# Performance work log

Hardware: AMD Instinct MI355X
Metric: run time of the kernel (lower is better)

## Reference

```python
import jax, jax.numpy as jnp
import numpy as np

NUM_NODES = 50000
NUM_EDGES = 800000
IN_CH = 64
OUT_CH = 64


def setup_inputs() -> dict:
    key = jax.random.key(0)
    k1, k2, k3, k4 = jax.random.split(key, 4)
    x = jax.random.normal(k1, (NUM_NODES, IN_CH), dtype=jnp.float32)
    edge_index = jax.random.randint(k2, (2, NUM_EDGES), 0, NUM_NODES, dtype=jnp.int32)
    W = jax.random.normal(k3, (IN_CH, OUT_CH), dtype=jnp.float32) * 0.05
    b = jax.random.normal(k4, (OUT_CH,), dtype=jnp.float32) * 0.05
    return {"x": x, "edge_index": edge_index, "W": W, "b": b}


def reference(x, edge_index, W, b):
    row, col = edge_index[0], edge_index[1]
    # Stage 1: in-degree of target nodes (math of one-hot sum == segment count)
    deg = jax.ops.segment_sum(jnp.ones_like(col, dtype=jnp.float32), col,
                              num_segments=NUM_NODES)
    deg_inv_sqrt = jnp.where(deg > 0, (deg + 1e-16) ** -0.5, 0.0)
    norm = deg_inv_sqrt[row] * deg_inv_sqrt[col]          # [E]
    # Stage 2+3: gather source features and scale by edge norm
    msg = norm[:, None] * x[row]                          # [E, IN_CH]
    # Stage 4: scatter-sum into target nodes (math of one-hot matmul)
    agg = jax.ops.segment_sum(msg, col, num_segments=NUM_NODES)  # [N, IN_CH]
    # Stage 5+6: linear transform + ReLU
    return jax.nn.relu(agg @ W + b)                       # [N, OUT_CH]
```

## Files before the change

kernel.cpp:

```cpp
#include <hip/hip_runtime.h>
#include <hip/hip_fp16.h>


#define C_CH 64
#define BW   128
#define BSH  7
#define MAXBUK 512
#define BIN_CHUNK 2048
#define NPB  32

__global__ void clearcur_kernel(int* __restrict__ bcur, int nbuk) {
    int i = blockIdx.x * blockDim.x + threadIdx.x;
    if (i < nbuk) bcur[i] = 0;
}

__global__ void __launch_bounds__(256)
bin_kernel(const int* __restrict__ row, const int* __restrict__ col,
           int* __restrict__ bcur, unsigned* __restrict__ epk,
           int E, int nbuk, int cap) {
    __shared__ int h[MAXBUK];
    __shared__ int rb[MAXBUK];
    __shared__ unsigned short rank[BIN_CHUNK];
    int tid = threadIdx.x;
    int e0 = blockIdx.x * BIN_CHUNK;
    int cntE = E - e0; if (cntE > BIN_CHUNK) cntE = BIN_CHUNK;

    for (int i = tid; i < nbuk; i += 256) h[i] = 0;
    __syncthreads();

    const int4* col4 = (const int4*)(col + e0);
    const int4* row4 = (const int4*)(row + e0);
    int cnt4 = cntE >> 2;
    for (int i = tid; i < cnt4; i += 256) {
        int4 c = col4[i];
        rank[4*i+0] = (unsigned short)atomicAdd(&h[c.x >> BSH], 1);
        rank[4*i+1] = (unsigned short)atomicAdd(&h[c.y >> BSH], 1);
        rank[4*i+2] = (unsigned short)atomicAdd(&h[c.z >> BSH], 1);
        rank[4*i+3] = (unsigned short)atomicAdd(&h[c.w >> BSH], 1);
    }
    for (int i = (cnt4 << 2) + tid; i < cntE; i += 256)
        rank[i] = (unsigned short)atomicAdd(&h[col[e0 + i] >> BSH], 1);
    __syncthreads();

    for (int i = tid; i < nbuk; i += 256)
        rb[i] = h[i] ? atomicAdd(&bcur[i], h[i]) : 0;
    __syncthreads();

    for (int i = tid; i < cnt4; i += 256) {
        int4 c = col4[i];
        int4 r = row4[i];
        #pragma unroll
        for (int j = 0; j < 4; ++j) {
            int cc = (j == 0) ? c.x : (j == 1) ? c.y : (j == 2) ? c.z : c.w;
            int rr = (j == 0) ? r.x : (j == 1) ? r.y : (j == 2) ? r.z : r.w;
            int bkt = cc >> BSH;
            int rel = rb[bkt] + (int)rank[4*i+j];
            if (rel < cap)
                epk[bkt * cap + rel] = ((unsigned)(cc & (BW - 1)) << 16) | (unsigned)rr;
        }
    }
    for (int i = (cnt4 << 2) + tid; i < cntE; i += 256) {
        int cc = col[e0 + i];
        int bkt = cc >> BSH;
        int rel = rb[bkt] + (int)rank[i];
        if (rel < cap)
            epk[bkt * cap + rel] = ((unsigned)(cc & (BW - 1)) << 16) | (unsigned)row[e0 + i];
    }
}

__global__ void __launch_bounds__(512)
build_kernel(const unsigned* __restrict__ epk, const int* __restrict__ bcur,
             const float* __restrict__ x,
             int4* __restrict__ seg,
             unsigned short* __restrict__ srcs, __half* __restrict__ xsh,
             int N, int cap) {
    __shared__ int cnt[BW];
    __shared__ int sc[BW];
    __shared__ int cur[BW];
    __shared__ float dv[BW];
    __shared__ int tot;
    __shared__ unsigned short sl[4096];
    int tid = threadIdx.x;
    int b   = blockIdx.x;
    int base = b * cap;
    int cb = bcur[b]; if (cb > cap) cb = cap;
    int nb0 = b << BSH;
    int nn  = N - nb0; if (nn > BW) nn = BW;

    if (tid < BW) cnt[tid] = 0;
    for (int i = tid; i < cap; i += 512)
        sl[i] = (unsigned short)N;
    __syncthreads();
    for (int i = tid; i < cb; i += 512)
        atomicAdd(&cnt[epk[base + i] >> 16], 1);
    __syncthreads();
    if (tid < BW) sc[tid] = (cnt[tid] + 7) & ~7;
    __syncthreads();
    for (int off = 1; off < BW; off <<= 1) {
        int t = (tid < BW && tid >= off) ? sc[tid - off] : 0;
        __syncthreads();
        if (tid < BW) sc[tid] += t;
        __syncthreads();
    }
    if (tid < BW) {
        int d  = cnt[tid];
        int dp = (d + 7) & ~7;
        int ex = sc[tid] - dp;
        cur[tid] = ex;
        if (tid == BW - 1) tot = sc[tid];
        if (tid < nn) {
            float di = (d > 0) ? rsqrtf((float)d) : 0.0f;
            dv[tid] = di;
            seg[nb0 + tid] = make_int4(base + ex, d, __float_as_int(di), 0);
        }
    }
    __syncthreads();
    for (int i = tid; i < cb; i += 512) {
        unsigned p = epk[base + i];
        int pos = atomicAdd(&cur[p >> 16], 1);
        if (pos < cap) sl[pos] = (unsigned short)(p & 0xFFFFu);
    }
    __syncthreads();
    int cbp = tot; if (cbp > cap) cbp = cap;
    for (int i = tid; i < cbp; i += 512)
        srcs[base + i] = sl[i];

    int tot2 = nn * (C_CH / 2);
    const float2* x2 = (const float2*)x;
    __half2* o2 = (__half2*)xsh;
    for (int i = tid; i < tot2; i += 512) {
        int nl = i >> 5;
        int c2 = i & 31;
        long long gi = (long long)(nb0 + nl) * (C_CH / 2) + c2;
        float2 v = x2[gi];
        float dn = dv[nl];
        o2[gi] = __floats2half2_rn(v.x * dn, v.y * dn);
    }
    if (b == 0 && tid < C_CH / 2)
        o2[(long long)N * (C_CH / 2) + tid] = __floats2half2_rn(0.0f, 0.0f);
}

__global__ void __launch_bounds__(512)
gather_kernel(const uint2* __restrict__ xsh8,
              const unsigned short* __restrict__ srcs,
              const int4* __restrict__ seg,
              const float* __restrict__ W, const float* __restrict__ b,
              float* __restrict__ out, int N) {
    __shared__ float Ws[C_CH * C_CH];
    __shared__ float bs[C_CH];
    __shared__ float ags[NPB][68];

    int tid = threadIdx.x;
    {
        const float4* W4 = (const float4*)W;
        float4* Ws4 = (float4*)Ws;
        for (int i = tid; i < C_CH * C_CH / 4; i += 512) Ws4[i] = W4[i];
        if (tid < C_CH) bs[tid] = b[tid];
    }

    int g  = tid >> 4;
    int c4 = tid & 15;
    int t = blockIdx.x * NPB + g;

    if (t < N) {
        float4 acc = make_float4(0.f, 0.f, 0.f, 0.f);
        int4 sg = seg[t];
        int s0 = sg.x;
        int degp = (sg.y + 7) & ~7;
        for (int eb = 0; eb < degp; eb += 8) {
            uint4 sv = *(const uint4*)(srcs + s0 + eb);
            int r0 = (int)(sv.x & 0xFFFFu), r1 = (int)(sv.x >> 16);
            int r2 = (int)(sv.y & 0xFFFFu), r3 = (int)(sv.y >> 16);
            int r4 = (int)(sv.z & 0xFFFFu), r5 = (int)(sv.z >> 16);
            int r6 = (int)(sv.w & 0xFFFFu), r7 = (int)(sv.w >> 16);
            uint2 u0 = xsh8[r0 * 16 + c4];
            uint2 u1 = xsh8[r1 * 16 + c4];
            uint2 u2 = xsh8[r2 * 16 + c4];
            uint2 u3 = xsh8[r3 * 16 + c4];
            uint2 u4 = xsh8[r4 * 16 + c4];
            uint2 u5 = xsh8[r5 * 16 + c4];
            uint2 u6 = xsh8[r6 * 16 + c4];
            uint2 u7 = xsh8[r7 * 16 + c4];
            #pragma unroll
            for (int k = 0; k < 8; ++k) {
                uint2 u = (k==0)?u0:(k==1)?u1:(k==2)?u2:(k==3)?u3:
                          (k==4)?u4:(k==5)?u5:(k==6)?u6:u7;
                float2 f0 = __half22float2(*(__half2*)&u.x);
                float2 f1 = __half22float2(*(__half2*)&u.y);
                acc.x += f0.x; acc.y += f0.y; acc.z += f1.x; acc.w += f1.y;
            }
        }
        float dt = __int_as_float(sg.z);
        acc.x *= dt; acc.y *= dt; acc.z *= dt; acc.w *= dt;
        *(float4*)&ags[g][4 * c4] = acc;
    }
    __syncthreads();

    if (t < N) {
        float4 o = *(const float4*)&bs[4 * c4];
        #pragma unroll
        for (int kq = 0; kq < C_CH / 4; ++kq) {
            float4 a4 = *(const float4*)&ags[g][4 * kq];
            float4 w0 = *(const float4*)&Ws[(4 * kq + 0) * C_CH + 4 * c4];
            float4 w1 = *(const float4*)&Ws[(4 * kq + 1) * C_CH + 4 * c4];
            float4 w2 = *(const float4*)&Ws[(4 * kq + 2) * C_CH + 4 * c4];
            float4 w3 = *(const float4*)&Ws[(4 * kq + 3) * C_CH + 4 * c4];
            o.x = fmaf(a4.x, w0.x, o.x); o.y = fmaf(a4.x, w0.y, o.y);
            o.z = fmaf(a4.x, w0.z, o.z); o.w = fmaf(a4.x, w0.w, o.w);
            o.x = fmaf(a4.y, w1.x, o.x); o.y = fmaf(a4.y, w1.y, o.y);
            o.z = fmaf(a4.y, w1.z, o.z); o.w = fmaf(a4.y, w1.w, o.w);
            o.x = fmaf(a4.z, w2.x, o.x); o.y = fmaf(a4.z, w2.y, o.y);
            o.z = fmaf(a4.z, w2.z, o.z); o.w = fmaf(a4.z, w2.w, o.w);
            o.x = fmaf(a4.w, w3.x, o.x); o.y = fmaf(a4.w, w3.y, o.y);
            o.z = fmaf(a4.w, w3.z, o.z); o.w = fmaf(a4.w, w3.w, o.w);
        }
        o.x = fmaxf(o.x, 0.f); o.y = fmaxf(o.y, 0.f);
        o.z = fmaxf(o.z, 0.f); o.w = fmaxf(o.w, 0.f);
        *(float4*)&out[(long long)t * C_CH + 4 * c4] = o;
    }
}

extern "C" void kernel_launch(void* const* d_in, const int* in_sizes, int n_in,
                              void* d_out, int out_size, void* d_ws, size_t ws_size,
                              hipStream_t stream) {
    const float* x  = (const float*)d_in[0];
    const int*   ei = (const int*)  d_in[1];
    const float* W  = (const float*)d_in[2];
    const float* b  = (const float*)d_in[3];
    float* out = (float*)d_out;

    const int N = in_sizes[0] / C_CH;
    const int E = in_sizes[1] / 2;
    const int* row = ei;
    const int* col = ei + E;
    const int nbuk = (N + BW - 1) >> BSH;

    auto need = [&](int cap) {
        return (size_t)nbuk * cap * 6
             + (size_t)N * 16 + 256
             + (((size_t)nbuk * 4 + 127) & ~(size_t)127)
             + (size_t)(N + 1) * C_CH * 2;
    };
    int cap = 4096;
    if (ws_size < need(4096)) cap = 3072;

    char* ws = (char*)d_ws;
    unsigned* epk = (unsigned*)ws;      ws += (size_t)nbuk * cap * 4;
    unsigned short* srcs = (unsigned short*)ws;  ws += (size_t)nbuk * cap * 2;
    int4* seg = (int4*)ws;              ws += (size_t)N * 16;
    int* bcur = (int*)ws;               ws += ((size_t)nbuk * 4 + 127) & ~(size_t)127;
    __half* xsh = (__half*)ws;

    clearcur_kernel<<<(nbuk + 255) / 256, 256, 0, stream>>>(bcur, nbuk);
    bin_kernel <<<(E + BIN_CHUNK - 1) / BIN_CHUNK, 256, 0, stream>>>(row, col, bcur, epk, E, nbuk, cap);
    build_kernel<<<nbuk, 512, 0, stream>>>(epk, bcur, x, seg, srcs, xsh, N, cap);
    gather_kernel<<<(N + NPB - 1) / NPB, 512, 0, stream>>>((const uint2*)xsh, srcs, seg,
                                                           W, b, out, N);
}
```

Before: 56.12 us.

## Fuse CSR source-list construction into the gather kernel via shared memory

The per-bucket counting sort of source indices moves out of the build kernel and into the gather kernel, which rebuilds it in shared memory and then processes the bucket's 128 nodes in four rounds of 32. The build kernel now only computes degrees and writes the prescaled half-precision features. This removes the global srcs and seg arrays and their write/read round trip. In exchange the gather grid shrinks from about 1563 blocks to about 391 blocks with heavier per-block work and more syncs, and the epk histogram is computed twice, which may lower parallelism and occupancy.

```diff
diff --git a/kernel.cpp b/kernel.cpp
--- a/kernel.cpp
+++ b/kernel.cpp
@@ -7,7 +7,6 @@
 #define BSH  7
 #define MAXBUK 512
 #define BIN_CHUNK 2048
-#define NPB  32
 
 __global__ void clearcur_kernel(int* __restrict__ bcur, int nbuk) {
     int i = blockIdx.x * blockDim.x + threadIdx.x;
@@ -68,18 +67,12 @@
     }
 }
 
-__global__ void __launch_bounds__(512)
-build_kernel(const unsigned* __restrict__ epk, const int* __restrict__ bcur,
-             const float* __restrict__ x,
-             int4* __restrict__ seg,
-             unsigned short* __restrict__ srcs, __half* __restrict__ xsh,
-             int N, int cap) {
+__global__ void __launch_bounds__(256)
+build_lite_kernel(const unsigned* __restrict__ epk, const int* __restrict__ bcur,
+                  const float* __restrict__ x, __half* __restrict__ xsh,
+                  int N, int cap) {
     __shared__ int cnt[BW];
-    __shared__ int sc[BW];
-    __shared__ int cur[BW];
     __shared__ float dv[BW];
-    __shared__ int tot;
-    __shared__ unsigned short sl[4096];
     int tid = threadIdx.x;
     int b   = blockIdx.x;
     int base = b * cap;
@@ -88,47 +81,20 @@
     int nn  = N - nb0; if (nn > BW) nn = BW;
 
     if (tid < BW) cnt[tid] = 0;
-    for (int i = tid; i < cap; i += 512)
-        sl[i] = (unsigned short)N;
-    __syncthreads();
-    for (int i = tid; i < cb; i += 512)
-        atomicAdd(&cnt[epk[base + i] >> 16], 1);
-    __syncthreads();
-    if (tid < BW) sc[tid] = (cnt[tid] + 7) & ~7;
-    __syncthreads();
-    for (int off = 1; off < BW; off <<= 1) {
-        int t = (tid < BW && tid >= off) ? sc[tid - off] : 0;
-        __syncthreads();
-        if (tid < BW) sc[tid] += t;
-        __syncthreads();
-    }
-    if (tid < BW) {
-        int d  = cnt[tid];
-        int dp = (d + 7) & ~7;
-        int ex = sc[tid] - dp;
-        cur[tid] = ex;
-        if (tid == BW - 1) tot = sc[tid];
-        if (tid < nn) {
-            float di = (d > 0) ? rsqrtf((float)d) : 0.0f;
-            dv[tid] = di;
-            seg[nb0 + tid] = make_int4(base + ex, d, __float_as_int(di), 0);
-        }
-    }
-    __syncthreads();
-    for (int i = tid; i < cb; i += 512) {
-        unsigned p = epk[base + i];
-        int pos = atomicAdd(&cur[p >> 16], 1);
-        if (pos < cap) sl[pos] = (unsigned short)(p & 0xFFFFu);
-    }
-    __syncthreads();
-    int cbp = tot; if (cbp > cap) cbp = cap;
-    for (int i = tid; i < cbp; i += 512)
-        srcs[base + i] = sl[i];
+    __syncthreads();
+    for (int i = tid; i < cb; i += 256)
+        atomicAdd(&cnt[(epk[base + i] >> 16) & (BW - 1)], 1);
+    __syncthreads();
+    if (tid < nn) {
+        int d = cnt[tid];
+        dv[tid] = (d > 0) ? rsqrtf((float)d) : 0.0f;
+    }
+    __syncthreads();
 
     int tot2 = nn * (C_CH / 2);
     const float2* x2 = (const float2*)x;
     __half2* o2 = (__half2*)xsh;
-    for (int i = tid; i < tot2; i += 512) {
+    for (int i = tid; i < tot2; i += 256) {
         int nl = i >> 5;
         int c2 = i & 31;
         long long gi = (long long)(nb0 + nl) * (C_CH / 2) + c2;
@@ -141,82 +107,126 @@
 }
 
 __global__ void __launch_bounds__(512)
-gather_kernel(const uint2* __restrict__ xsh8,
-              const unsigned short* __restrict__ srcs,
-              const int4* __restrict__ seg,
-              const float* __restrict__ W, const float* __restrict__ b,
-              float* __restrict__ out, int N) {
+gather_fused_kernel(const uint2* __restrict__ xsh8,
+                    const unsigned* __restrict__ epk,
+                    const int* __restrict__ bcur,
+                    const float* __restrict__ W, const float* __restrict__ bvec,
+                    float* __restrict__ out, int N, int cap) {
     __shared__ float Ws[C_CH * C_CH];
     __shared__ float bs[C_CH];
-    __shared__ float ags[NPB][68];
+    __shared__ unsigned short sl[4096];
+    __shared__ int cnt[BW];
+    __shared__ int sc[BW];
+    __shared__ int cur[BW];
+    __shared__ int sstart[BW];
+    __shared__ float ags[32][68];
 
     int tid = threadIdx.x;
     {
         const float4* W4 = (const float4*)W;
         float4* Ws4 = (float4*)Ws;
         for (int i = tid; i < C_CH * C_CH / 4; i += 512) Ws4[i] = W4[i];
-        if (tid < C_CH) bs[tid] = b[tid];
-    }
+        if (tid < C_CH) bs[tid] = bvec[tid];
+    }
+    if (tid < BW) cnt[tid] = 0;
+    for (int i = tid; i < cap && i < 4096; i += 512)
+        sl[i] = (unsigned short)N;
+    __syncthreads();
+
+    int b = blockIdx.x;
+    int base = b * cap;
+    int cb = bcur[b]; if (cb > cap) cb = cap;
+    int nb0 = b << BSH;
+    int nn  = N - nb0; if (nn > BW) nn = BW;
+
+    for (int i = tid; i < cb; i += 512)
+        atomicAdd(&cnt[epk[base + i] >> 16], 1);
+    __syncthreads();
+    if (tid < BW) sc[tid] = (cnt[tid] + 7) & ~7;
+    __syncthreads();
+    for (int off = 1; off < BW; off <<= 1) {
+        int t = (tid < BW && tid >= off) ? sc[tid - off] : 0;
+        __syncthreads();
+        if (tid < BW) sc[tid] += t;
+        __syncthreads();
+    }
+    if (tid < BW) {
+        int d  = cnt[tid];
+        int dp = (d + 7) & ~7;
+        int ex = sc[tid] - dp;
+        cur[tid] = ex;
+        sstart[tid] = ex;
+    }
+    __syncthreads();
+    for (int i = tid; i < cb; i += 512) {
+        unsigned p = epk[base + i];
+        int pos = atomicAdd(&cur[p >> 16], 1);
+        if (pos < cap && pos < 4096) sl[pos] = (unsigned short)(p & 0xFFFFu);
+    }
+    __syncthreads();
 
     int g  = tid >> 4;
     int c4 = tid & 15;
-    int t = blockIdx.x * NPB + g;
-
-    if (t < N) {
-        float4 acc = make_float4(0.f, 0.f, 0.f, 0.f);
-        int4 sg = seg[t];
-        int s0 = sg.x;
-        int degp = (sg.y + 7) & ~7;
-        for (int eb = 0; eb < degp; eb += 8) {
-            uint4 sv = *(const uint4*)(srcs + s0 + eb);
-            int r0 = (int)(sv.x & 0xFFFFu), r1 = (int)(sv.x >> 16);
-            int r2 = (int)(sv.y & 0xFFFFu), r3 = (int)(sv.y >> 16);
-            int r4 = (int)(sv.z & 0xFFFFu), r5 = (int)(sv.z >> 16);
-            int r6 = (int)(sv.w & 0xFFFFu), r7 = (int)(sv.w >> 16);
-            uint2 u0 = xsh8[r0 * 16 + c4];
-            uint2 u1 = xsh8[r1 * 16 + c4];
-            uint2 u2 = xsh8[r2 * 16 + c4];
-            uint2 u3 = xsh8[r3 * 16 + c4];
-            uint2 u4 = xsh8[r4 * 16 + c4];
-            uint2 u5 = xsh8[r5 * 16 + c4];
-            uint2 u6 = xsh8[r6 * 16 + c4];
-            uint2 u7 = xsh8[r7 * 16 + c4];
+    #pragma unroll 1
+    for (int rrd = 0; rrd < 4; ++rrd) {
+        int v = rrd * 32 + g;
+        bool act = (v < nn);
+        if (act) {
+            float4 acc = make_float4(0.f, 0.f, 0.f, 0.f);
+            int s0 = sstart[v];
+            int d  = cnt[v];
+            int degp = (d + 7) & ~7;
+            for (int eb = 0; eb < degp; eb += 8) {
+                uint4 sv = *(const uint4*)(sl + s0 + eb);
+                int r0 = (int)(sv.x & 0xFFFFu), r1 = (int)(sv.x >> 16);
+                int r2 = (int)(sv.y & 0xFFFFu), r3 = (int)(sv.y >> 16);
+                int r4 = (int)(sv.z & 0xFFFFu), r5 = (int)(sv.z >> 16);
+                int r6 = (int)(sv.w & 0xFFFFu), r7 = (int)(sv.w >> 16);
+                uint2 u0 = xsh8[r0 * 16 + c4];
+                uint2 u1 = xsh8[r1 * 16 + c4];
+                uint2 u2 = xsh8[r2 * 16 + c4];
+                uint2 u3 = xsh8[r3 * 16 + c4];
+                uint2 u4 = xsh8[r4 * 16 + c4];
+                uint2 u5 = xsh8[r5 * 16 + c4];
+                uint2 u6 = xsh8[r6 * 16 + c4];
+                uint2 u7 = xsh8[r7 * 16 + c4];
+                #pragma unroll
+                for (int k = 0; k < 8; ++k) {
+                    uint2 u = (k==0)?u0:(k==1)?u1:(k==2)?u2:(k==3)?u3:
+                              (k==4)?u4:(k==5)?u5:(k==6)?u6:u7;
+                    float2 f0 = __half22float2(*(__half2*)&u.x);
+                    float2 f1 = __half22float2(*(__half2*)&u.y);
+                    acc.x += f0.x; acc.y += f0.y; acc.z += f1.x; acc.w += f1.y;
+                }
+            }
+            float dt = (d > 0) ? rsqrtf((float)d) : 0.0f;
+            acc.x *= dt; acc.y *= dt; acc.z *= dt; acc.w *= dt;
+            *(float4*)&ags[g][4 * c4] = acc;
+        }
+        __syncthreads();
+        if (act) {
+            float4 o = *(const float4*)&bs[4 * c4];
             #pragma unroll
-            for (int k = 0; k < 8; ++k) {
-                uint2 u = (k==0)?u0:(k==1)?u1:(k==2)?u2:(k==3)?u3:
-                          (k==4)?u4:(k==5)?u5:(k==6)?u6:u7;
-                float2 f0 = __half22float2(*(__half2*)&u.x);
-                float2 f1 = __half22float2(*(__half2*)&u.y);
-                acc.x += f0.x; acc.y += f0.y; acc.z += f1.x; acc.w += f1.y;
+            for (int kq = 0; kq < C_CH / 4; ++kq) {
+                float4 a4 = *(const float4*)&ags[g][4 * kq];
+                float4 w0 = *(const float4*)&Ws[(4 * kq + 0) * C_CH + 4 * c4];
+                float4 w1 = *(const float4*)&Ws[(4 * kq + 1) * C_CH + 4 * c4];
+                float4 w2 = *(const float4*)&Ws[(4 * kq + 2) * C_CH + 4 * c4];
+                float4 w3 = *(const float4*)&Ws[(4 * kq + 3) * C_CH + 4 * c4];
+                o.x = fmaf(a4.x, w0.x, o.x); o.y = fmaf(a4.x, w0.y, o.y);
+                o.z = fmaf(a4.x, w0.z, o.z); o.w = fmaf(a4.x, w0.w, o.w);
+                o.x = fmaf(a4.y, w1.x, o.x); o.y = fmaf(a4.y, w1.y, o.y);
+                o.z = fmaf(a4.y, w1.z, o.z); o.w = fmaf(a4.y, w1.w, o.w);
+                o.x = fmaf(a4.z, w2.x, o.x); o.y = fmaf(a4.z, w2.y, o.y);
+                o.z = fmaf(a4.z, w2.z, o.z); o.w = fmaf(a4.z, w2.w, o.w);
+                o.x = fmaf(a4.w, w3.x, o.x); o.y = fmaf(a4.w, w3.y, o.y);
+                o.z = fmaf(a4.w, w3.z, o.z); o.w = fmaf(a4.w, w3.w, o.w);
             }
+            o.x = fmaxf(o.x, 0.f); o.y = fmaxf(o.y, 0.f);
+            o.z = fmaxf(o.z, 0.f); o.w = fmaxf(o.w, 0.f);
+            *(float4*)&out[(long long)(nb0 + v) * C_CH + 4 * c4] = o;
         }
-        float dt = __int_as_float(sg.z);
-        acc.x *= dt; acc.y *= dt; acc.z *= dt; acc.w *= dt;
-        *(float4*)&ags[g][4 * c4] = acc;
-    }
-    __syncthreads();
-
-    if (t < N) {
-        float4 o = *(const float4*)&bs[4 * c4];
-        #pragma unroll
-        for (int kq = 0; kq < C_CH / 4; ++kq) {
-            float4 a4 = *(const float4*)&ags[g][4 * kq];
-            float4 w0 = *(const float4*)&Ws[(4 * kq + 0) * C_CH + 4 * c4];
-            float4 w1 = *(const float4*)&Ws[(4 * kq + 1) * C_CH + 4 * c4];
-            float4 w2 = *(const float4*)&Ws[(4 * kq + 2) * C_CH + 4 * c4];
-            float4 w3 = *(const float4*)&Ws[(4 * kq + 3) * C_CH + 4 * c4];
-            o.x = fmaf(a4.x, w0.x, o.x); o.y = fmaf(a4.x, w0.y, o.y);
-            o.z = fmaf(a4.x, w0.z, o.z); o.w = fmaf(a4.x, w0.w, o.w);
-            o.x = fmaf(a4.y, w1.x, o.x); o.y = fmaf(a4.y, w1.y, o.y);
-            o.z = fmaf(a4.y, w1.z, o.z); o.w = fmaf(a4.y, w1.w, o.w);
-            o.x = fmaf(a4.z, w2.x, o.x); o.y = fmaf(a4.z, w2.y, o.y);
-            o.z = fmaf(a4.z, w2.z, o.z); o.w = fmaf(a4.z, w2.w, o.w);
-            o.x = fmaf(a4.w, w3.x, o.x); o.y = fmaf(a4.w, w3.y, o.y);
-            o.z = fmaf(a4.w, w3.z, o.z); o.w = fmaf(a4.w, w3.w, o.w);
-        }
-        o.x = fmaxf(o.x, 0.f); o.y = fmaxf(o.y, 0.f);
-        o.z = fmaxf(o.z, 0.f); o.w = fmaxf(o.w, 0.f);
-        *(float4*)&out[(long long)t * C_CH + 4 * c4] = o;
+        __syncthreads();
     }
 }
 
@@ -236,8 +246,7 @@
     const int nbuk = (N + BW - 1) >> BSH;
 
     auto need = [&](int cap) {
-        return (size_t)nbuk * cap * 6
-             + (size_t)N * 16 + 256
+        return (size_t)nbuk * cap * 4
              + (((size_t)nbuk * 4 + 127) & ~(size_t)127)
              + (size_t)(N + 1) * C_CH * 2;
     };
@@ -246,14 +255,12 @@
 
     char* ws = (char*)d_ws;
     unsigned* epk = (unsigned*)ws;      ws += (size_t)nbuk * cap * 4;
-    unsigned short* srcs = (unsigned short*)ws;  ws += (size_t)nbuk * cap * 2;
-    int4* seg = (int4*)ws;              ws += (size_t)N * 16;
     int* bcur = (int*)ws;               ws += ((size_t)nbuk * 4 + 127) & ~(size_t)127;
     __half* xsh = (__half*)ws;
 
-    clearcur_kernel<<<(nbuk + 255) / 256, 256, 0, stream>>>(bcur, nbuk);
-    bin_kernel <<<(E + BIN_CHUNK - 1) / BIN_CHUNK, 256, 0, stream>>>(row, col, bcur, epk, E, nbuk, cap);
-    build_kernel<<<nbuk, 512, 0, stream>>>(epk, bcur, x, seg, srcs, xsh, N, cap);
-    gather_kernel<<<(N + NPB - 1) / NPB, 512, 0, stream>>>((const uint2*)xsh, srcs, seg,
-                                                           W, b, out, N);
-}
+    clearcur_kernel   <<<(nbuk + 255) / 256, 256, 0, stream>>>(bcur, nbuk);
+    bin_kernel        <<<(E + BIN_CHUNK - 1) / BIN_CHUNK, 256, 0, stream>>>(row, col, bcur, epk, E, nbuk, cap);
+    build_lite_kernel <<<nbuk, 256, 0, stream>>>(epk, bcur, x, xsh, N, cap);
+    gather_fused_kernel<<<nbuk, 512, 0, stream>>>((const uint2*)xsh, epk, bcur,
+                                                  W, b, out, N, cap);
+}
```

Result: slower. 62.63 us (+11.6%).
